# Kernel tuning notes

Measured on AMD Instinct MI355X. Metric: run time of the kernel, lower is better.

Reference implementation:

```python
import jax, jax.numpy as jnp
import numpy as np
import math

EMBED_DIM = 1024
NUM_HEADS = 16
HEAD_DIM = EMBED_DIM // NUM_HEADS


def setup_inputs() -> dict:
    key = jax.random.key(0)
    ks = jax.random.split(key, 12)
    B, N = 2, 2048
    s = 1.0 / math.sqrt(EMBED_DIM)
    inp = {
        "query": jax.random.normal(ks[0], (B, N, EMBED_DIM), jnp.float32),
        "key": jax.random.normal(ks[1], (B, N, EMBED_DIM), jnp.float32),
        "value": jax.random.normal(ks[2], (B, N, EMBED_DIM), jnp.float32),
        "Wq": jax.random.normal(ks[3], (EMBED_DIM, EMBED_DIM), jnp.float32) * s,
        "bq": jnp.zeros((EMBED_DIM,), jnp.float32),
        "Wk": jax.random.normal(ks[4], (EMBED_DIM, EMBED_DIM), jnp.float32) * s,
        "bk": jnp.zeros((EMBED_DIM,), jnp.float32),
        "Wv": jax.random.normal(ks[5], (EMBED_DIM, EMBED_DIM), jnp.float32) * s,
        "bv": jnp.zeros((EMBED_DIM,), jnp.float32),
        "Wo": jax.random.normal(ks[6], (EMBED_DIM, EMBED_DIM), jnp.float32) * s,
        "bo": jnp.zeros((EMBED_DIM,), jnp.float32),
        "gate": jnp.zeros((NUM_HEADS,), jnp.float32),
    }
    return inp


def reference(query, key, value, Wq, bq, Wk, bk, Wv, bv, Wo, bo, gate):
    B, Nq, _ = query.shape
    Nk = key.shape[1]
    H, D = NUM_HEADS, HEAD_DIM
    # projections (Linear: x @ W.T + b); split heads -> [B, H, N, D]
    q = (query @ Wq.T + bq).reshape(B, Nq, H, D).transpose(0, 2, 1, 3)
    k = (key @ Wk.T + bk).reshape(B, Nk, H, D).transpose(0, 2, 1, 3)
    v = (value @ Wv.T + bv).reshape(B, Nk, H, D).transpose(0, 2, 1, 3)
    # scaled logits with per-head sigmoid gate folded into the scale
    scale = jax.nn.sigmoid(gate) / math.sqrt(D)  # [H]
    logits = jnp.einsum("bhqd,bhkd->bhqk", q, k) * scale[None, :, None, None]
    attn = jax.nn.softmax(logits, axis=-1)
    out = jnp.einsum("bhqk,bhkd->bhqd", attn, v)
    out = out.transpose(0, 2, 1, 3).reshape(B, Nq, H * D)
    return out @ Wo.T + bo
```

## Files before the change

### kernel.cpp

```cpp
#include <hip/hip_runtime.h>
#include <hip/hip_bf16.h>
#include <cstdint>


#define DEV __device__ __forceinline__
typedef __attribute__((ext_vector_type(8))) short bf16x8;
typedef __attribute__((ext_vector_type(4))) float f32x4;
typedef unsigned short u16;

DEV void async16(const void* g, void* l) {
  __builtin_amdgcn_global_load_lds(
      (const __attribute__((address_space(1))) unsigned int*)g,
      (__attribute__((address_space(3))) unsigned int*)l, 16, 0, 0);
}

DEV u16 bf16_rne(float f) {
  unsigned int u = __builtin_bit_cast(unsigned int, f);
  u += 0x7FFFu + ((u >> 16) & 1u);
  return (u16)(u >> 16);
}

DEV u16 cvt16(float x) {
  __hip_bfloat16 h = __float2bfloat16(x);
  return __builtin_bit_cast(u16, h);
}

DEV unsigned cvtpk(float lo, float hi) {
  unsigned r;
  asm("v_cvt_pk_bf16_f32 %0, %1, %2" : "=v"(r) : "v"(lo), "v"(hi));
  return r;
}

__global__ __launch_bounds__(256) void cast_all(
    const float* __restrict__ q, const float* __restrict__ k, const float* __restrict__ v,
    const float* __restrict__ Wq, const float* __restrict__ Wk,
    const float* __restrict__ Wv, const float* __restrict__ Wo,
    u16* __restrict__ XQ, u16* __restrict__ XK, u16* __restrict__ XV,
    u16* __restrict__ WQB, u16* __restrict__ WKB, u16* __restrict__ WVB,
    u16* __restrict__ WOB) {
  int idx = blockIdx.x * 256 + threadIdx.x;
  const float* src; u16* dst; int i;
  if      (idx <  524288) { src = q;  dst = XQ;  i = idx; }
  else if (idx < 1048576) { src = k;  dst = XK;  i = idx -  524288; }
  else if (idx < 1572864) { src = v;  dst = XV;  i = idx - 1048576; }
  else if (idx < 1703936) { src = Wq; dst = WQB; i = idx - 1572864; }
  else if (idx < 1835008) { src = Wk; dst = WKB; i = idx - 1703936; }
  else if (idx < 1966080) { src = Wv; dst = WVB; i = idx - 1835008; }
  else                    { src = Wo; dst = WOB; i = idx - 1966080; }
  const float4* p = (const float4*)src + (size_t)i * 2;
  float4 a = p[0], b = p[1];
  union { u16 us[8]; uint4 vv; } u;
  u.us[0] = bf16_rne(a.x); u.us[1] = bf16_rne(a.y);
  u.us[2] = bf16_rne(a.z); u.us[3] = bf16_rne(a.w);
  u.us[4] = bf16_rne(b.x); u.us[5] = bf16_rne(b.y);
  u.us[6] = bf16_rne(b.z); u.us[7] = bf16_rne(b.w);
  ((uint4*)dst)[i] = u.vv;
}

__global__ __launch_bounds__(256, 3) void gemm_qkv(
    const u16* __restrict__ XQ, const u16* __restrict__ XK, const u16* __restrict__ XV,
    const u16* __restrict__ Wb,
    const float* __restrict__ bq, const float* __restrict__ bkb, const float* __restrict__ bv,
    const float* __restrict__ gate,
    u16* __restrict__ QB, u16* __restrict__ KB, u16* __restrict__ VTB) {
  __shared__ __attribute__((aligned(16))) u16 As[2][128 * 32];
  __shared__ __attribute__((aligned(16))) u16 Bs[2][128 * 32];
  const int t = threadIdx.x, lane = t & 63, w = t >> 6;
  const int l15 = lane & 15, quad = lane >> 4;
  const int xcd = blockIdx.x & 7, idx = blockIdx.x >> 3;
  const int seg = idx >> 5, r5 = idx & 31;
  const int bm = (xcd << 2) + (r5 >> 3), bn = r5 & 7;
  const int m0 = bm << 7, n0 = bn << 7;
  const u16* A = (seg == 0) ? XQ : (seg == 1) ? XK : XV;
  const u16* W = Wb + (long)seg * 1048576;
  const int wm = (w >> 1) << 6, wn = (w & 1) << 6;
  const int r0 = t >> 2, cc0 = (t & 3) * 8;
  const u16* gA0 = A + (long)(m0 + r0) * 1024 + cc0;
  const u16* gA1 = gA0 + 64 * 1024;
  const u16* gB0 = W + (long)(n0 + r0) * 1024 + cc0;
  const u16* gB1 = gB0 + 64 * 1024;

  async16(gA0, &As[0][t * 8]); async16(gA1, &As[0][(t + 256) * 8]);
  async16(gB0, &Bs[0][t * 8]); async16(gB1, &Bs[0][(t + 256) * 8]);

  f32x4 acc[4][4] = {};
  for (int k0 = 0; k0 < 1024; k0 += 32) {
    const int cur = (k0 >> 5) & 1;
    __syncthreads();
    if (k0 + 32 < 1024) {
      const int kn = k0 + 32, nb = cur ^ 1;
      async16(gA0 + kn, &As[nb][t * 8]); async16(gA1 + kn, &As[nb][(t + 256) * 8]);
      async16(gB0 + kn, &Bs[nb][t * 8]); async16(gB1 + kn, &Bs[nb][(t + 256) * 8]);
    }
    bf16x8 af[4], bfm[4];
#pragma unroll
    for (int i = 0; i < 4; i++)
      af[i] = *(const bf16x8*)&As[cur][(wm + i * 16 + l15) * 32 + quad * 8];
#pragma unroll
    for (int j = 0; j < 4; j++)
      bfm[j] = *(const bf16x8*)&Bs[cur][(wn + j * 16 + l15) * 32 + quad * 8];
#pragma unroll
    for (int i = 0; i < 4; i++)
#pragma unroll
      for (int j = 0; j < 4; j++)
        acc[i][j] = __builtin_amdgcn_mfma_f32_16x16x32_bf16(af[i], bfm[j], acc[i][j], 0, 0, 0);
  }

  if (seg == 2) {
#pragma unroll
    for (int i = 0; i < 4; i++) {
      int token = m0 + wm + i * 16 + quad * 4;
      int bb_ = token >> 11, n = token & 2047;
#pragma unroll
      for (int j = 0; j < 4; j++) {
        int col = n0 + wn + j * 16 + l15;
        float bb = bv[col];
        union { u16 us[4]; uint2 u2; } pk;
#pragma unroll
        for (int r = 0; r < 4; r++) pk.us[r] = bf16_rne(acc[i][j][r] + bb);
        *(uint2*)&VTB[(long)(bb_ * 1024 + col) * 2048 + n] = pk.u2;
      }
    }
  } else {
    const float* bias = seg ? bkb : bq;
    u16* C = seg ? KB : QB;
#pragma unroll
    for (int j = 0; j < 4; j++) {
      int col = n0 + wn + j * 16 + l15;
      float bb = bias[col];
      float scl = 1.f;
      if (seg == 0) {
        float g = gate[col >> 6];
        float sig = 1.f / (1.f + __builtin_amdgcn_exp2f(-g * 1.44269504f));
        scl = sig * 0.125f * 1.44269504f;
      }
#pragma unroll
      for (int i = 0; i < 4; i++) {
        int row = m0 + wm + i * 16 + quad * 4;
#pragma unroll
        for (int r = 0; r < 4; r++)
          C[(long)(row + r) * 1024 + col] = bf16_rne((acc[i][j][r] + bb) * scl);
      }
    }
  }
}

__global__ __launch_bounds__(256, 2) void gemm_out(
    const u16* __restrict__ A, const u16* __restrict__ W,
    const float* __restrict__ bias, float* __restrict__ Cf) {
  __shared__ __attribute__((aligned(16))) u16 As[2][64 * 32];
  __shared__ __attribute__((aligned(16))) u16 Bs[2][128 * 32];
  const int t = threadIdx.x, lane = t & 63, w = t >> 6;
  const int l15 = lane & 15, quad = lane >> 4;
  const int xcd = blockIdx.x & 7, idx = blockIdx.x >> 3;
  const int bm = (xcd << 3) + (idx >> 3), bn = idx & 7;
  const int m0 = bm << 6, n0 = bn << 7;
  const int wm = (w >> 1) << 5, wn = (w & 1) << 6;
  const int r0 = t >> 2, cc0 = (t & 3) * 8;
  const u16* gA = A + (long)(m0 + r0) * 1024 + cc0;
  const u16* gB0 = W + (long)(n0 + r0) * 1024 + cc0;
  const u16* gB1 = gB0 + 64 * 1024;

  async16(gA, &As[0][t * 8]);
  async16(gB0, &Bs[0][t * 8]); async16(gB1, &Bs[0][(t + 256) * 8]);

  f32x4 acc[2][4] = {};
  for (int k0 = 0; k0 < 1024; k0 += 32) {
    const int cur = (k0 >> 5) & 1;
    __syncthreads();
    if (k0 + 32 < 1024) {
      const int kn = k0 + 32, nb = cur ^ 1;
      async16(gA + kn, &As[nb][t * 8]);
      async16(gB0 + kn, &Bs[nb][t * 8]); async16(gB1 + kn, &Bs[nb][(t + 256) * 8]);
    }
    bf16x8 af[2], bfm[4];
#pragma unroll
    for (int i = 0; i < 2; i++)
      af[i] = *(const bf16x8*)&As[cur][(wm + i * 16 + l15) * 32 + quad * 8];
#pragma unroll
    for (int j = 0; j < 4; j++)
      bfm[j] = *(const bf16x8*)&Bs[cur][(wn + j * 16 + l15) * 32 + quad * 8];
#pragma unroll
    for (int i = 0; i < 2; i++)
#pragma unroll
      for (int j = 0; j < 4; j++)
        acc[i][j] = __builtin_amdgcn_mfma_f32_16x16x32_bf16(af[i], bfm[j], acc[i][j], 0, 0, 0);
  }

#pragma unroll
  for (int j = 0; j < 4; j++) {
    int col = n0 + wn + j * 16 + l15;
    float bb = bias[col];
#pragma unroll
    for (int i = 0; i < 2; i++) {
      int row = m0 + wm + i * 16 + quad * 4;
#pragma unroll
      for (int r = 0; r < 4; r++)
        Cf[(long)(row + r) * 1024 + col] = acc[i][j][r] + bb;
    }
  }
}

__global__ __launch_bounds__(256, 4) void attn_kernel(
    const u16* __restrict__ Q, const u16* __restrict__ Kb,
    const u16* __restrict__ Vt, u16* __restrict__ Op0, u16* __restrict__ Op3,
    float* __restrict__ lp) {
  __shared__ __attribute__((aligned(16))) u16 Ks[2][32 * 64];
  __shared__ __attribute__((aligned(16))) u16 Vs[2][64 * 32];
  const int t = threadIdx.x, lane = t & 63, w = t >> 6;
  const int l15 = lane & 15, quad = lane >> 4;
  const int xcd = blockIdx.x & 7, rr = blockIdx.x >> 3;
  const int ksp = xcd >> 1, qt = ((xcd & 1) << 3) | rr;
  const int h = blockIdx.y, b = blockIdx.z;
  const int q0 = qt * 128, tok0 = b * 2048, key0 = ksp * 512;
  const u16* Kbase = Kb + (long)tok0 * 1024 + h * 64;
  const u16* Vbase = Vt + (long)(b * 1024 + h * 64) * 2048 + key0;

  bf16x8 aq[2][2];
#pragma unroll
  for (int i = 0; i < 2; i++) {
    long row = tok0 + q0 + w * 32 + i * 16 + l15;
#pragma unroll
    for (int ks = 0; ks < 2; ks++)
      aq[i][ks] = *(const bf16x8*)&Q[row * 1024 + h * 64 + ks * 32 + quad * 8];
  }

  const int rk = t >> 3, ck = t & 7;
  const int rv = t >> 2, cv = t & 3;
  const u16* kg = Kbase + (long)(key0 + rk) * 1024 + ((ck ^ ((rk >> 1) & 7)) * 8);
  const u16* vg = Vbase + (long)rv * 2048 + ((cv ^ ((rv >> 1) & 3)) * 8);
  u16* ksd = &Ks[0][t * 8];
  u16* vsd = &Vs[0][t * 8];

  auto STAGE = [&](int tk, int bu) {
    async16(kg + (long)tk * 32768, ksd + bu * 2048);
    async16(vg + tk * 32, vsd + bu * 2048);
  };

  STAGE(0, 0);

  float l_st[2] = {};
  f32x4 O[2][4] = {};

  for (int kt = 0; kt < 16; kt++) {
    const int cur = kt & 1;
    __syncthreads();
    if (kt + 1 < 16) STAGE(kt + 1, cur ^ 1);

    f32x4 s[2][2] = {};
    __builtin_amdgcn_s_setprio(1);
#pragma unroll
    for (int ks = 0; ks < 2; ks++) {
      bf16x8 bk_[2];
#pragma unroll
      for (int j = 0; j < 2; j++) {
        int rl = 2 * l15 + j;
        bk_[j] = *(const bf16x8*)&Ks[cur][rl * 64 + (((ks * 4 + quad) ^ (l15 & 7))) * 8];
      }
#pragma unroll
      for (int i = 0; i < 2; i++)
#pragma unroll
        for (int j = 0; j < 2; j++)
          s[i][j] = __builtin_amdgcn_mfma_f32_16x16x32_bf16(bk_[j], aq[i][ks], s[i][j], 0, 0, 0);
    }
    __builtin_amdgcn_s_setprio(0);

    bf16x8 ap[2];
#pragma unroll
    for (int i = 0; i < 2; i++) {
      union { unsigned uw[4]; bf16x8 v8; } pw;
#pragma unroll
      for (int r = 0; r < 4; r++) {
        float p0 = __builtin_amdgcn_exp2f(s[i][0][r]);
        float p1 = __builtin_amdgcn_exp2f(s[i][1][r]);
        l_st[i] += p0 + p1;
        pw.uw[r] = cvtpk(p0, p1);
      }
      ap[i] = pw.v8;
    }

    bf16x8 bv_[4];
#pragma unroll
    for (int dj = 0; dj < 4; dj++) {
      int rl = dj * 16 + l15;
      bv_[dj] = *(const bf16x8*)&Vs[cur][rl * 32 + ((quad ^ ((rl >> 1) & 3))) * 8];
    }
    __builtin_amdgcn_s_setprio(1);
#pragma unroll
    for (int i = 0; i < 2; i++)
#pragma unroll
      for (int dj = 0; dj < 4; dj++)
        O[i][dj] = __builtin_amdgcn_mfma_f32_16x16x32_bf16(ap[i], bv_[dj], O[i][dj], 0, 0, 0);
    __builtin_amdgcn_s_setprio(0);
  }

  u16* dst = (ksp == 3) ? Op3 : (Op0 + (long)ksp * 4194304);
#pragma unroll
  for (int i = 0; i < 2; i++) {
    float ls = l_st[i];
    ls += __shfl_xor(ls, 16); ls += __shfl_xor(ls, 32);
    if (quad == 0) {
      long qrow = tok0 + q0 + w * 32 + i * 16 + l15;
      lp[ksp * 65536 + (int)qrow * 16 + h] = ls;
    }
#pragma unroll
    for (int r = 0; r < 4; r++) {
      long row = tok0 + q0 + w * 32 + i * 16 + quad * 4 + r;
#pragma unroll
      for (int dj = 0; dj < 4; dj++)
        dst[row * 1024 + h * 64 + dj * 16 + l15] = cvt16(O[i][dj][r]);
    }
  }
}

__global__ __launch_bounds__(256) void merge_kernel(
    const u16* __restrict__ Op0, const u16* __restrict__ Op3,
    const float* __restrict__ lp, u16* __restrict__ AO) {
  int idx = blockIdx.x * 256 + threadIdx.x;
  int tok = idx >> 7, rem = idx & 127, h = rem >> 3;
  int li = tok * 16 + h;
  float inv = 1.f / (lp[li] + lp[65536 + li] + lp[131072 + li] + lp[196608 + li]);
  union U { uint4 v; u16 us[8]; };
  U a0, a1, a2, a3, uo;
  a0.v = ((const uint4*)Op0)[idx];
  a1.v = ((const uint4*)Op0)[idx + 524288];
  a2.v = ((const uint4*)Op0)[idx + 1048576];
  a3.v = ((const uint4*)Op3)[idx];
#pragma unroll
  for (int j = 0; j < 8; j++) {
    float f0 = __builtin_bit_cast(float, (unsigned)((unsigned)a0.us[j] << 16));
    float f1 = __builtin_bit_cast(float, (unsigned)((unsigned)a1.us[j] << 16));
    float f2 = __builtin_bit_cast(float, (unsigned)((unsigned)a2.us[j] << 16));
    float f3 = __builtin_bit_cast(float, (unsigned)((unsigned)a3.us[j] << 16));
    uo.us[j] = cvt16((f0 + f1 + f2 + f3) * inv);
  }
  ((uint4*)AO)[idx] = uo.v;
}

extern "C" void kernel_launch(void* const* d_in, const int* in_sizes, int n_in,
                              void* d_out, int out_size, void* d_ws, size_t ws_size,
                              hipStream_t stream) {
  const float* q  = (const float*)d_in[0];
  const float* k  = (const float*)d_in[1];
  const float* v  = (const float*)d_in[2];
  const float* Wq = (const float*)d_in[3];
  const float* bq = (const float*)d_in[4];
  const float* Wk = (const float*)d_in[5];
  const float* bk = (const float*)d_in[6];
  const float* Wv = (const float*)d_in[7];
  const float* bv = (const float*)d_in[8];
  const float* Wo = (const float*)d_in[9];
  const float* bo = (const float*)d_in[10];
  const float* gate = (const float*)d_in[11];
  float* out = (float*)d_out;
  char* ws = (char*)d_ws;

  const size_t MB = 1u << 20;
  u16* WQB = (u16*)(ws + 0 * MB);
  u16* WKB = (u16*)(ws + 2 * MB);
  u16* WVB = (u16*)(ws + 4 * MB);
  u16* WOB = (u16*)(ws + 6 * MB);
  u16* XQ  = (u16*)(ws + 8 * MB);
  u16* XK  = (u16*)(ws + 16 * MB);
  u16* XV  = (u16*)(ws + 24 * MB);
  u16* QB  = (u16*)(ws + 32 * MB);
  u16* KB  = (u16*)(ws + 40 * MB);
  u16* OPp  = (u16*)(ws + 8 * MB);
  u16* OPd3 = (u16*)((char*)d_out + 8 * MB);
  float* LP = (float*)(ws + 0 * MB);
  u16* AOB  = (u16*)(ws + 8 * MB);
  u16* VTB  = (u16*)d_out;

  cast_all<<<8192, 256, 0, stream>>>(q, k, v, Wq, Wk, Wv, Wo,
                                     XQ, XK, XV, WQB, WKB, WVB, WOB);
  gemm_qkv<<<768, 256, 0, stream>>>(XQ, XK, XV, WQB, bq, bk, bv, gate, QB, KB, VTB);
  attn_kernel<<<dim3(64, 16, 2), 256, 0, stream>>>(QB, KB, VTB, OPp, OPd3, LP);
  merge_kernel<<<2048, 256, 0, stream>>>(OPp, OPd3, LP, AOB);
  gemm_out<<<512, 256, 0, stream>>>(AOB, WOB, bo, out);
}
```

Before: 228.0 us.

## Fuse activation fp32-to-bf16 cast into QKV GEMM loads and retile output GEMM

The QKV projection GEMM now loads fp32 activations straight into registers, converts them to bf16 and writes them to LDS with a register prefetch one stage ahead. This removes the separate cast pass over q/k/v and its bf16 round-trip through global memory, so only the weights are still cast up front. The output GEMM moves to 64x64 tiles with twice as many blocks and higher occupancy. The cost is that the A-operand loads become synchronous register loads instead of async global-to-LDS copies, which adds register pressure in gemm_qkv.

```diff
diff --git a/kernel.cpp b/kernel.cpp
--- a/kernel.cpp
+++ b/kernel.cpp
@@ -31,34 +31,32 @@
   return r;
 }
 
-__global__ __launch_bounds__(256) void cast_all(
-    const float* __restrict__ q, const float* __restrict__ k, const float* __restrict__ v,
+DEV uint4 cvt8(float4 a, float4 b) {
+  union { u16 us[8]; uint4 v; } u;
+  u.us[0] = bf16_rne(a.x); u.us[1] = bf16_rne(a.y);
+  u.us[2] = bf16_rne(a.z); u.us[3] = bf16_rne(a.w);
+  u.us[4] = bf16_rne(b.x); u.us[5] = bf16_rne(b.y);
+  u.us[6] = bf16_rne(b.z); u.us[7] = bf16_rne(b.w);
+  return u.v;
+}
+
+__global__ __launch_bounds__(256) void cast_w(
     const float* __restrict__ Wq, const float* __restrict__ Wk,
     const float* __restrict__ Wv, const float* __restrict__ Wo,
-    u16* __restrict__ XQ, u16* __restrict__ XK, u16* __restrict__ XV,
     u16* __restrict__ WQB, u16* __restrict__ WKB, u16* __restrict__ WVB,
     u16* __restrict__ WOB) {
   int idx = blockIdx.x * 256 + threadIdx.x;
   const float* src; u16* dst; int i;
-  if      (idx <  524288) { src = q;  dst = XQ;  i = idx; }
-  else if (idx < 1048576) { src = k;  dst = XK;  i = idx -  524288; }
-  else if (idx < 1572864) { src = v;  dst = XV;  i = idx - 1048576; }
-  else if (idx < 1703936) { src = Wq; dst = WQB; i = idx - 1572864; }
-  else if (idx < 1835008) { src = Wk; dst = WKB; i = idx - 1703936; }
-  else if (idx < 1966080) { src = Wv; dst = WVB; i = idx - 1835008; }
-  else                    { src = Wo; dst = WOB; i = idx - 1966080; }
+  if      (idx < 131072) { src = Wq; dst = WQB; i = idx; }
+  else if (idx < 262144) { src = Wk; dst = WKB; i = idx - 131072; }
+  else if (idx < 393216) { src = Wv; dst = WVB; i = idx - 262144; }
+  else                   { src = Wo; dst = WOB; i = idx - 393216; }
   const float4* p = (const float4*)src + (size_t)i * 2;
-  float4 a = p[0], b = p[1];
-  union { u16 us[8]; uint4 vv; } u;
-  u.us[0] = bf16_rne(a.x); u.us[1] = bf16_rne(a.y);
-  u.us[2] = bf16_rne(a.z); u.us[3] = bf16_rne(a.w);
-  u.us[4] = bf16_rne(b.x); u.us[5] = bf16_rne(b.y);
-  u.us[6] = bf16_rne(b.z); u.us[7] = bf16_rne(b.w);
-  ((uint4*)dst)[i] = u.vv;
+  ((uint4*)dst)[i] = cvt8(p[0], p[1]);
 }
 
 __global__ __launch_bounds__(256, 3) void gemm_qkv(
-    const u16* __restrict__ XQ, const u16* __restrict__ XK, const u16* __restrict__ XV,
+    const float* __restrict__ Xq, const float* __restrict__ Xk, const float* __restrict__ Xv,
     const u16* __restrict__ Wb,
     const float* __restrict__ bq, const float* __restrict__ bkb, const float* __restrict__ bv,
     const float* __restrict__ gate,
@@ -71,17 +69,30 @@
   const int seg = idx >> 5, r5 = idx & 31;
   const int bm = (xcd << 2) + (r5 >> 3), bn = r5 & 7;
   const int m0 = bm << 7, n0 = bn << 7;
-  const u16* A = (seg == 0) ? XQ : (seg == 1) ? XK : XV;
+  const float* A = (seg == 0) ? Xq : (seg == 1) ? Xk : Xv;
   const u16* W = Wb + (long)seg * 1048576;
   const int wm = (w >> 1) << 6, wn = (w & 1) << 6;
   const int r0 = t >> 2, cc0 = (t & 3) * 8;
-  const u16* gA0 = A + (long)(m0 + r0) * 1024 + cc0;
-  const u16* gA1 = gA0 + 64 * 1024;
+  const float* gA0 = A + (long)(m0 + r0) * 1024 + cc0;
+  const float* gA1 = gA0 + 64 * 1024;
   const u16* gB0 = W + (long)(n0 + r0) * 1024 + cc0;
   const u16* gB1 = gB0 + 64 * 1024;
 
-  async16(gA0, &As[0][t * 8]); async16(gA1, &As[0][(t + 256) * 8]);
+  float4 ra0, ra1, ra2, ra3;
+  auto LOADA = [&](int ko) {
+    const float4* p0 = (const float4*)(gA0 + ko);
+    const float4* p1 = (const float4*)(gA1 + ko);
+    ra0 = p0[0]; ra1 = p0[1]; ra2 = p1[0]; ra3 = p1[1];
+  };
+  auto WRITEA = [&](int nb) {
+    *(uint4*)&As[nb][t * 8] = cvt8(ra0, ra1);
+    *(uint4*)&As[nb][(t + 256) * 8] = cvt8(ra2, ra3);
+  };
+
+  LOADA(0);
   async16(gB0, &Bs[0][t * 8]); async16(gB1, &Bs[0][(t + 256) * 8]);
+  WRITEA(0);
+  LOADA(32);
 
   f32x4 acc[4][4] = {};
   for (int k0 = 0; k0 < 1024; k0 += 32) {
@@ -89,8 +100,9 @@
     __syncthreads();
     if (k0 + 32 < 1024) {
       const int kn = k0 + 32, nb = cur ^ 1;
-      async16(gA0 + kn, &As[nb][t * 8]); async16(gA1 + kn, &As[nb][(t + 256) * 8]);
+      WRITEA(nb);
       async16(gB0 + kn, &Bs[nb][t * 8]); async16(gB1 + kn, &Bs[nb][(t + 256) * 8]);
+      if (k0 + 64 < 1024) LOADA(k0 + 64);
     }
     bf16x8 af[4], bfm[4];
 #pragma unroll
@@ -145,50 +157,49 @@
   }
 }
 
-__global__ __launch_bounds__(256, 2) void gemm_out(
+__global__ __launch_bounds__(256, 4) void gemm_out(
     const u16* __restrict__ A, const u16* __restrict__ W,
     const float* __restrict__ bias, float* __restrict__ Cf) {
   __shared__ __attribute__((aligned(16))) u16 As[2][64 * 32];
-  __shared__ __attribute__((aligned(16))) u16 Bs[2][128 * 32];
+  __shared__ __attribute__((aligned(16))) u16 Bs[2][64 * 32];
   const int t = threadIdx.x, lane = t & 63, w = t >> 6;
   const int l15 = lane & 15, quad = lane >> 4;
   const int xcd = blockIdx.x & 7, idx = blockIdx.x >> 3;
-  const int bm = (xcd << 3) + (idx >> 3), bn = idx & 7;
-  const int m0 = bm << 6, n0 = bn << 7;
-  const int wm = (w >> 1) << 5, wn = (w & 1) << 6;
+  const int bm = (xcd << 3) + (idx >> 4), bn = idx & 15;
+  const int m0 = bm << 6, n0 = bn << 6;
+  const int wm = (w >> 1) << 5, wn = (w & 1) << 5;
   const int r0 = t >> 2, cc0 = (t & 3) * 8;
   const u16* gA = A + (long)(m0 + r0) * 1024 + cc0;
-  const u16* gB0 = W + (long)(n0 + r0) * 1024 + cc0;
-  const u16* gB1 = gB0 + 64 * 1024;
+  const u16* gB = W + (long)(n0 + r0) * 1024 + cc0;
 
   async16(gA, &As[0][t * 8]);
-  async16(gB0, &Bs[0][t * 8]); async16(gB1, &Bs[0][(t + 256) * 8]);
-
-  f32x4 acc[2][4] = {};
+  async16(gB, &Bs[0][t * 8]);
+
+  f32x4 acc[2][2] = {};
   for (int k0 = 0; k0 < 1024; k0 += 32) {
     const int cur = (k0 >> 5) & 1;
     __syncthreads();
     if (k0 + 32 < 1024) {
       const int kn = k0 + 32, nb = cur ^ 1;
       async16(gA + kn, &As[nb][t * 8]);
-      async16(gB0 + kn, &Bs[nb][t * 8]); async16(gB1 + kn, &Bs[nb][(t + 256) * 8]);
-    }
-    bf16x8 af[2], bfm[4];
+      async16(gB + kn, &Bs[nb][t * 8]);
+    }
+    bf16x8 af[2], bfm[2];
 #pragma unroll
     for (int i = 0; i < 2; i++)
       af[i] = *(const bf16x8*)&As[cur][(wm + i * 16 + l15) * 32 + quad * 8];
 #pragma unroll
-    for (int j = 0; j < 4; j++)
+    for (int j = 0; j < 2; j++)
       bfm[j] = *(const bf16x8*)&Bs[cur][(wn + j * 16 + l15) * 32 + quad * 8];
 #pragma unroll
     for (int i = 0; i < 2; i++)
 #pragma unroll
-      for (int j = 0; j < 4; j++)
+      for (int j = 0; j < 2; j++)
         acc[i][j] = __builtin_amdgcn_mfma_f32_16x16x32_bf16(af[i], bfm[j], acc[i][j], 0, 0, 0);
   }
 
 #pragma unroll
-  for (int j = 0; j < 4; j++) {
+  for (int j = 0; j < 2; j++) {
     int col = n0 + wn + j * 16 + l15;
     float bb = bias[col];
 #pragma unroll
@@ -360,9 +371,6 @@
   u16* WKB = (u16*)(ws + 2 * MB);
   u16* WVB = (u16*)(ws + 4 * MB);
   u16* WOB = (u16*)(ws + 6 * MB);
-  u16* XQ  = (u16*)(ws + 8 * MB);
-  u16* XK  = (u16*)(ws + 16 * MB);
-  u16* XV  = (u16*)(ws + 24 * MB);
   u16* QB  = (u16*)(ws + 32 * MB);
   u16* KB  = (u16*)(ws + 40 * MB);
   u16* OPp  = (u16*)(ws + 8 * MB);
@@ -371,10 +379,9 @@
   u16* AOB  = (u16*)(ws + 8 * MB);
   u16* VTB  = (u16*)d_out;
 
-  cast_all<<<8192, 256, 0, stream>>>(q, k, v, Wq, Wk, Wv, Wo,
-                                     XQ, XK, XV, WQB, WKB, WVB, WOB);
-  gemm_qkv<<<768, 256, 0, stream>>>(XQ, XK, XV, WQB, bq, bk, bv, gate, QB, KB, VTB);
+  cast_w<<<2048, 256, 0, stream>>>(Wq, Wk, Wv, Wo, WQB, WKB, WVB, WOB);
+  gemm_qkv<<<768, 256, 0, stream>>>(q, k, v, WQB, bq, bk, bv, gate, QB, KB, VTB);
   attn_kernel<<<dim3(64, 16, 2), 256, 0, stream>>>(QB, KB, VTB, OPp, OPd3, LP);
   merge_kernel<<<2048, 256, 0, stream>>>(OPp, OPd3, LP, AOB);
-  gemm_out<<<512, 256, 0, stream>>>(AOB, WOB, bo, out);
-}
+  gemm_out<<<1024, 256, 0, stream>>>(AOB, WOB, bo, out);
+}
```

Result: no change. 227.1 us (-0.4%).
